# Optimization experiments

Hardware: AMD Instinct MI355X
Metric: run time of the kernel (lower is better)

The kernel has to match this reference:

```python
import jax, jax.numpy as jnp
import numpy as np

VOCAB = 32000
HID = 1024
HEADS = 16
HEAD_DIM = HID // HEADS
LAYERS = 8
INTER = 4 * HID
ROPE_BASE = 100000.0
EPS = 1e-5


def setup_inputs() -> dict:
    key = jax.random.key(0)
    ks = jax.random.split(key, 12)
    s = 0.02
    inp = {
        'input_ids': jax.random.randint(ks[0], (2, 2048), 0, VOCAB),
        'embed_W': jax.random.normal(ks[1], (VOCAB, HID), jnp.float32) * s,
        'Wq': jax.random.normal(ks[2], (LAYERS, HID, HID), jnp.float32) * s,
        'Wk': jax.random.normal(ks[3], (LAYERS, HID, HID), jnp.float32) * s,
        'Wv': jax.random.normal(ks[4], (LAYERS, HID, HID), jnp.float32) * s,
        'Wo': jax.random.normal(ks[5], (LAYERS, HID, HID), jnp.float32) * s,
        'Wg': jax.random.normal(ks[6], (LAYERS, HID, INTER), jnp.float32) * s,
        'Wu': jax.random.normal(ks[7], (LAYERS, HID, INTER), jnp.float32) * s,
        'Wd': jax.random.normal(ks[8], (LAYERS, INTER, HID), jnp.float32) * s,
        'norm1_w': jnp.ones((LAYERS, HID), jnp.float32),
        'norm2_w': jnp.ones((LAYERS, HID), jnp.float32),
        'final_norm_w': jnp.ones((HID,), jnp.float32),
        'head_W': jax.random.normal(ks[9], (HID, VOCAB), jnp.float32) * s,
    }
    return inp


def rms_norm(x, w):
    return x * jax.lax.rsqrt(jnp.mean(x * x, axis=-1, keepdims=True) + EPS) * w


def rope_tables(seq_len):
    freq = 1.0 / (ROPE_BASE ** (jnp.arange(0, HEAD_DIM, 2, dtype=jnp.float32) / HEAD_DIM))
    ang = jnp.arange(seq_len, dtype=jnp.float32)[:, None] * freq  # [S, d/2]
    cos = jnp.concatenate([jnp.cos(ang), jnp.cos(ang)], axis=-1)  # [S, d]
    sin = jnp.concatenate([jnp.sin(ang), jnp.sin(ang)], axis=-1)
    return cos, sin


def rotate_half(x):
    h = x.shape[-1] // 2
    return jnp.concatenate([-x[..., h:], x[..., :h]], axis=-1)


def apply_rope(q, k, cos, sin):
    # q,k: [B,S,H,D]; cos,sin: [S,D] -> broadcast over heads via [:,None,:]
    c = cos[:, None, :]
    s = sin[:, None, :]
    return q * c + rotate_half(q) * s, k * c + rotate_half(k) * s


def attention(x, wq, wk, wv, wo, cos, sin, causal_mask):
    B, S, _ = x.shape
    q = (x @ wq).reshape(B, S, HEADS, HEAD_DIM)
    k = (x @ wk).reshape(B, S, HEADS, HEAD_DIM)
    v = (x @ wv).reshape(B, S, HEADS, HEAD_DIM)
    q, k = apply_rope(q, k, cos, sin)
    scores = jnp.einsum('bqhd,bkhd->bhqk', q, k) / np.sqrt(HEAD_DIM)
    scores = jnp.clip(scores, -1000.0, 1000.0)
    scores = jnp.where(causal_mask, jnp.finfo(scores.dtype).min, scores)
    w = jax.nn.softmax(scores.astype(jnp.float32), axis=-1).astype(q.dtype)
    w = jnp.clip(w, 0.0, 1.0)
    ctx = jnp.einsum('bhqk,bkhd->bqhd', w, v).reshape(B, S, HID)
    return ctx @ wo


def reference(input_ids, embed_W, Wq, Wk, Wv, Wo, Wg, Wu, Wd, norm1_w, norm2_w, final_norm_w, head_W):
    B, S = input_ids.shape
    h = embed_W[input_ids]  # [B,S,HID]
    cos, sin = rope_tables(S)
    causal_mask = jnp.triu(jnp.ones((S, S), bool), k=1)[None, None]
    for l in range(LAYERS):
        h = h + attention(rms_norm(h, norm1_w[l]), Wq[l], Wk[l], Wv[l], Wo[l], cos, sin, causal_mask)
        hn = rms_norm(h, norm2_w[l])
        h = h + (jax.nn.silu(hn @ Wg[l]) * (hn @ Wu[l])) @ Wd[l]
    h = rms_norm(h, final_norm_w)
    logits = h @ head_W
    return logits, h
```

## Files before the change

### kernel.cpp

```cpp
#include <hip/hip_runtime.h>

#define T_TOK 4096
#define SEQ   2048
#define HID   1024
#define NH    16
#define HD    64
#define INTER 4096
#define NLAYER 8
#define VOCAB 32000

typedef short short8 __attribute__((ext_vector_type(8)));
typedef float f32x4  __attribute__((ext_vector_type(4)));

__device__ __forceinline__ unsigned short f2bf(float f){
  unsigned int u = __builtin_bit_cast(unsigned int, f);
  u += 0x7fffu + ((u >> 16) & 1u);
  return (unsigned short)(u >> 16);
}
__device__ __forceinline__ float bf2f(unsigned short b){
  unsigned int u = ((unsigned int)b) << 16;
  return __builtin_bit_cast(float, u);
}

#define GLOAD_LDS16(gsrc, ldst) \
  __builtin_amdgcn_global_load_lds((const __attribute__((address_space(1))) void*)(gsrc), \
                                   (__attribute__((address_space(3))) void*)(ldst), 16, 0, 0)

__global__ __launch_bounds__(256) void embed_kernel(const int* __restrict__ ids,
                                                    const float* __restrict__ W,
                                                    float* __restrict__ h){
  int i = blockIdx.x * 256 + threadIdx.x;
  int t = i >> 8, c = i & 255;
  ((float4*)h)[i] = ((const float4*)(W + (size_t)ids[t] * HID))[c];
}

__global__ __launch_bounds__(256) void rope_tab_kernel(float* __restrict__ cosT,
                                                       float* __restrict__ sinT){
  int i = blockIdx.x * 256 + threadIdx.x;
  int s = i >> 5, f = i & 31;
  float inv = expf(-((2.0f * (float)f) / 64.0f) * logf(100000.0f));
  float ang = (float)s * inv;
  cosT[i] = cosf(ang);
  sinT[i] = sinf(ang);
}

__global__ __launch_bounds__(256) void rmsnorm_kernel(const float* __restrict__ h,
                                                      const float* __restrict__ w,
                                                      unsigned short* __restrict__ out,
                                                      float* hcopy){
  int t = blockIdx.x, tid = threadIdx.x;
  float4 v = ((const float4*)(h + (size_t)t * HID))[tid];
  float ss = v.x*v.x + v.y*v.y + v.z*v.z + v.w*v.w;
  #pragma unroll
  for (int m = 1; m < 64; m <<= 1) ss += __shfl_xor(ss, m);
  __shared__ float red[4];
  if ((tid & 63) == 0) red[tid >> 6] = ss;
  __syncthreads();
  float r = rsqrtf((red[0] + red[1] + red[2] + red[3]) * (1.0f / HID) + 1e-5f);
  float4 wv = ((const float4*)w)[tid];
  float nx = v.x * r * wv.x;
  float ny = v.y * r * wv.y;
  float nz = v.z * r * wv.z;
  float nw = v.w * r * wv.w;
  ushort4 o;
  o.x = f2bf(nx); o.y = f2bf(ny); o.z = f2bf(nz); o.w = f2bf(nw);
  ((ushort4*)(out + (size_t)t * HID))[tid] = o;
  if (hcopy){
    float4 hv; hv.x = nx; hv.y = ny; hv.z = nz; hv.w = nw;
    ((float4*)(hcopy + (size_t)t * HID))[tid] = hv;
  }
}

__global__ __launch_bounds__(256) void rope_kernel(unsigned short* __restrict__ q,
                                                   unsigned short* __restrict__ k,
                                                   const float* __restrict__ cosT,
                                                   const float* __restrict__ sinT){
  int i = blockIdx.x * 256 + threadIdx.x;
  int t = i >> 9, rem = i & 511;
  int hh = rem >> 5, f = rem & 31;
  int s = t & (SEQ - 1);
  float c = cosT[s * 32 + f], sn = sinT[s * 32 + f];
  size_t base = (size_t)t * HID + hh * HD + f;
  float q0 = bf2f(q[base]), q1 = bf2f(q[base + 32]);
  q[base]      = f2bf((q0 * c - q1 * sn) * 0.125f);
  q[base + 32] = f2bf((q1 * c + q0 * sn) * 0.125f);
  float k0 = bf2f(k[base]), k1 = bf2f(k[base + 32]);
  k[base]      = f2bf(k0 * c - k1 * sn);
  k[base + 32] = f2bf(k1 * c + k0 * sn);
}

__global__ __launch_bounds__(256) void convert_w_swz(const float* __restrict__ W,
                                                     unsigned short* __restrict__ Wt,
                                                     int K, int N){
  __shared__ unsigned short t_lds[64][72];
  W  += (size_t)blockIdx.z * K * N;
  Wt += (size_t)blockIdx.z * K * N;
  const int n0 = blockIdx.x * 64, k0 = blockIdx.y * 64;
  const int tid = threadIdx.x;
  const int tr = tid >> 4, tc = tid & 15;
  #pragma unroll
  for (int i = 0; i < 4; ++i){
    int kk = tr + i * 16;
    float4 v = *(const float4*)(W + (size_t)(k0 + kk) * N + n0 + tc * 4);
    t_lds[tc*4+0][kk] = f2bf(v.x);
    t_lds[tc*4+1][kk] = f2bf(v.y);
    t_lds[tc*4+2][kk] = f2bf(v.z);
    t_lds[tc*4+3][kk] = f2bf(v.w);
  }
  __syncthreads();
  const int n = tid >> 2, cp = tid & 3;
  #pragma unroll
  for (int j = 0; j < 2; ++j){
    int c = cp * 2 + j;
    uint4 d = *(const uint4*)(&t_lds[n][c * 8]);
    *(uint4*)(Wt + (size_t)(n0 + n) * K + k0 + ((c ^ (n & 7)) << 3)) = d;
  }
}

__global__ __launch_bounds__(256) void convert_w_lin(const float* __restrict__ W,
                                                     unsigned short* __restrict__ Wt,
                                                     int K, int N){
  __shared__ unsigned short t_lds[64][72];
  const int n0 = blockIdx.x * 64, k0 = blockIdx.y * 64;
  const int tid = threadIdx.x;
  const int tr = tid >> 4, tc = tid & 15;
  #pragma unroll
  for (int i = 0; i < 4; ++i){
    int kk = tr + i * 16;
    float4 v = *(const float4*)(W + (size_t)(k0 + kk) * N + n0 + tc * 4);
    t_lds[tc*4+0][kk] = f2bf(v.x);
    t_lds[tc*4+1][kk] = f2bf(v.y);
    t_lds[tc*4+2][kk] = f2bf(v.z);
    t_lds[tc*4+3][kk] = f2bf(v.w);
  }
  __syncthreads();
  const int n = tid >> 2, cp = tid & 3;
  #pragma unroll
  for (int j = 0; j < 2; ++j){
    int c = cp * 2 + j;
    uint4 d = *(const uint4*)(&t_lds[n][c * 8]);
    *(uint4*)(Wt + (size_t)(n0 + n) * K + k0 + c * 8) = d;
  }
}

__device__ __forceinline__ void gemm_core64(const unsigned short* __restrict__ A,
                                            const unsigned short* __restrict__ Bt,
                                            int K, int m0, int n0,
                                            unsigned short* As, unsigned short* Bs,
                                            f32x4 (&acc)[4][4]){
  const int tid = threadIdx.x;
  const int lane = tid & 63, w = tid >> 6;
  const int l15 = lane & 15, g = lane >> 4;
  const int lr = lane >> 3;
  const int lc = lane & 7;
  const int wr = w >> 1, wc = w & 1;
  const int axor = ((lc ^ lr) << 3);

  #pragma unroll
  for (int m = 0; m < 4; ++m)
    #pragma unroll
    for (int n = 0; n < 4; ++n)
      #pragma unroll
      for (int i = 0; i < 4; ++i) acc[m][n][i] = 0.0f;

  for (int kk = 0; kk < K; kk += 64){
    __syncthreads();
    #pragma unroll
    for (int i = 0; i < 4; ++i){
      int rb = (i * 4 + w) * 8;
      GLOAD_LDS16(A  + (size_t)(m0 + rb + lr) * K + kk + axor,      As + rb * 64);
      GLOAD_LDS16(Bt + (size_t)(n0 + rb + lr) * K + kk + (lc << 3), Bs + rb * 64);
    }
    __syncthreads();
    short8 a[4][2], b[4][2];
    const int x = l15 & 7;
    #pragma unroll
    for (int m = 0; m < 4; ++m){
      int row = wr * 64 + m * 16 + l15;
      a[m][0] = *(const short8*)(As + row * 64 + ((g       ^ x) << 3));
      a[m][1] = *(const short8*)(As + row * 64 + (((4 + g) ^ x) << 3));
    }
    #pragma unroll
    for (int n = 0; n < 4; ++n){
      int row = wc * 64 + n * 16 + l15;
      b[n][0] = *(const short8*)(Bs + row * 64 + ((g       ^ x) << 3));
      b[n][1] = *(const short8*)(Bs + row * 64 + (((4 + g) ^ x) << 3));
    }
    #pragma unroll
    for (int m = 0; m < 4; ++m)
      #pragma unroll
      for (int n = 0; n < 4; ++n){
        acc[m][n] = __builtin_amdgcn_mfma_f32_16x16x32_bf16(a[m][0], b[n][0], acc[m][n], 0, 0, 0);
        acc[m][n] = __builtin_amdgcn_mfma_f32_16x16x32_bf16(a[m][1], b[n][1], acc[m][n], 0, 0, 0);
      }
  }
}

__device__ __forceinline__ void gemm_core32(const unsigned short* __restrict__ A,
                                            const unsigned short* __restrict__ Bt,
                                            int K, int m0, int n0,
                                            unsigned short* As, unsigned short* Bs,
                                            f32x4 (&acc)[4][4]){
  const int tid = threadIdx.x;
  const int lane = tid & 63, w = tid >> 6;
  const int l15 = lane & 15, g = lane >> 4;
  const int wr = w >> 1, wc = w & 1;
  const int srow = lane >> 2;
  const int schunk = (((lane & 3) ^ ((srow >> 1) & 3)) << 3);
  const int sx = (l15 >> 1) & 3;

  #pragma unroll
  for (int m = 0; m < 4; ++m)
    #pragma unroll
    for (int n = 0; n < 4; ++n)
      #pragma unroll
      for (int i = 0; i < 4; ++i) acc[m][n][i] = 0.0f;

  for (int kk = 0; kk < K; kk += 32){
    __syncthreads();
    GLOAD_LDS16(A  + (size_t)(m0 +      w*16 + srow) * K + kk + schunk, As + (w*16) * 32);
    GLOAD_LDS16(A  + (size_t)(m0 + 64 + w*16 + srow) * K + kk + schunk, As + (64 + w*16) * 32);
    GLOAD_LDS16(Bt + (size_t)(n0 +      w*16 + srow) * K + kk + schunk, Bs + (w*16) * 32);
    GLOAD_LDS16(Bt + (size_t)(n0 + 64 + w*16 + srow) * K + kk + schunk, Bs + (64 + w*16) * 32);
    __syncthreads();
    short8 a[4], b[4];
    #pragma unroll
    for (int m = 0; m < 4; ++m)
      a[m] = *(const short8*)(As + (wr*64 + m*16 + l15) * 32 + ((g ^ sx) << 3));
    #pragma unroll
    for (int n = 0; n < 4; ++n)
      b[n] = *(const short8*)(Bs + (wc*64 + n*16 + l15) * 32 + ((g ^ sx) << 3));
    #pragma unroll
    for (int m = 0; m < 4; ++m)
      #pragma unroll
      for (int n = 0; n < 4; ++n)
        acc[m][n] = __builtin_amdgcn_mfma_f32_16x16x32_bf16(a[m], b[n], acc[m][n], 0, 0, 0);
  }
}

template<int MODE>
__device__ __forceinline__ void gemm_epi(const f32x4 (&acc)[4][4], void* Cout,
                                         const float* __restrict__ resid,
                                         int N, int m0, int n0, int ldt){
  const int tid = threadIdx.x;
  const int lane = tid & 63, w = tid >> 6;
  const int l15 = lane & 15, g = lane >> 4;
  const int wr = w >> 1, wc = w & 1;
  #pragma unroll
  for (int m = 0; m < 4; ++m){
    #pragma unroll
    for (int n = 0; n < 4; ++n){
      int row0 = m0 + wr * 64 + m * 16 + g * 4;
      int col  = n0 + wc * 64 + n * 16 + l15;
      #pragma unroll
      for (int i = 0; i < 4; ++i){
        float v = acc[m][n][i];
        if (MODE == 0){
          ((unsigned short*)Cout)[(size_t)(row0 + i) * N + col] = f2bf(v);
        } else if (MODE == 1){
          size_t idx = (size_t)(row0 + i) * N + col;
          ((float*)Cout)[idx] = resid[idx] + v;
        } else if (MODE == 2){
          ((unsigned short*)Cout)[(size_t)col * ldt + (row0 + i)] = f2bf(v);
        } else {
          __builtin_nontemporal_store(v, &((float*)Cout)[(size_t)(row0 + i) * N + col]);
        }
      }
    }
  }
}

template<int MODE>
__global__ __launch_bounds__(256) void gemm64_k(const unsigned short* __restrict__ A,
                                                const unsigned short* __restrict__ Bt,
                                                void* Cout, const float* resid,
                                                int K, int N, int ldt){
  __shared__ unsigned short As[128 * 64];
  __shared__ unsigned short Bs[128 * 64];
  f32x4 acc[4][4];
  gemm_core64(A, Bt, K, blockIdx.x * 128, blockIdx.y * 128, As, Bs, acc);
  gemm_epi<MODE>(acc, Cout, resid, N, blockIdx.x * 128, blockIdx.y * 128, ldt);
}

__global__ __launch_bounds__(256) void gemm_qkv(const unsigned short* __restrict__ A,
                                                const unsigned short* __restrict__ BtQ,
                                                const unsigned short* __restrict__ BtK,
                                                const unsigned short* __restrict__ BtV,
                                                unsigned short* qb, unsigned short* kb,
                                                unsigned short* vt){
  __shared__ unsigned short As[128 * 64];
  __shared__ unsigned short Bs[128 * 64];
  const int nb = blockIdx.y, sel = nb >> 3, n0 = (nb & 7) * 128;
  const unsigned short* Bt = (sel == 0) ? BtQ : (sel == 1) ? BtK : BtV;
  f32x4 acc[4][4];
  gemm_core64(A, Bt, HID, blockIdx.x * 128, n0, As, Bs, acc);
  if (sel == 0)      gemm_epi<0>(acc, qb, nullptr, HID, blockIdx.x * 128, n0, 0);
  else if (sel == 1) gemm_epi<0>(acc, kb, nullptr, HID, blockIdx.x * 128, n0, 0);
  else               gemm_epi<2>(acc, vt, nullptr, HID, blockIdx.x * 128, n0, T_TOK);
}

__global__ __launch_bounds__(256) void gemm_gu(const unsigned short* __restrict__ A,
                                               const unsigned short* __restrict__ BtG,
                                               const unsigned short* __restrict__ BtU,
                                               unsigned short* gb, unsigned short* ub){
  __shared__ unsigned short As[128 * 64];
  __shared__ unsigned short Bs[128 * 64];
  const int nb = blockIdx.y, sel = nb >> 5, n0 = (nb & 31) * 128;
  f32x4 acc[4][4];
  gemm_core64(A, sel ? BtU : BtG, HID, blockIdx.x * 128, n0, As, Bs, acc);
  gemm_epi<0>(acc, sel ? ub : gb, nullptr, INTER, blockIdx.x * 128, n0, 0);
}

__global__ __launch_bounds__(256) void gemm_head(const unsigned short* __restrict__ A,
                                                 const unsigned short* __restrict__ Bt,
                                                 float* __restrict__ out){
  __shared__ unsigned short As[128 * 32];
  __shared__ unsigned short Bs[128 * 32];
  const int m0 = blockIdx.y * 128, n0 = blockIdx.x * 128;
  f32x4 acc[4][4];
  gemm_core32(A, Bt, HID, m0, n0, As, Bs, acc);
  gemm_epi<3>(acc, out, nullptr, VOCAB, m0, n0, 0);
}

__global__ __launch_bounds__(256, 2) void gemm_f32b(const unsigned short* __restrict__ A,
                                                    const float* __restrict__ Bw,
                                                    float* __restrict__ Cout,
                                                    int M, int N, int K){
  __shared__ unsigned short As[128 * 32];
  __shared__ unsigned short Bs[128 * 32];
  const int tid = threadIdx.x;
  const int lane = tid & 63, wid = tid >> 6;
  const int l15 = lane & 15, g = lane >> 4;
  const int wr = wid >> 1, wc = wid & 1;
  const int m0 = blockIdx.x * 128, n0 = blockIdx.y * 128;
  const int bcol = tid & 127, bhalf = tid >> 7;
  f32x4 acc[4][4];
  #pragma unroll
  for (int m = 0; m < 4; ++m)
    #pragma unroll
    for (int n = 0; n < 4; ++n)
      #pragma unroll
      for (int i = 0; i < 4; ++i) acc[m][n][i] = 0.0f;
  for (int kk = 0; kk < K; kk += 32){
    __syncthreads();
    #pragma unroll
    for (int cc = 0; cc < 2; ++cc){
      int c = tid + cc * 256;
      int row = c >> 2, kc = (c & 3) << 3;
      uint4 d = *(const uint4*)(A + (size_t)(m0 + row) * K + kk + kc);
      *(uint4*)(&As[row * 32 + kc]) = d;
    }
    {
      const float* bp = Bw + (size_t)(kk + bhalf * 16) * N + n0 + bcol;
      float f[16];
      #pragma unroll
      for (int j = 0; j < 16; ++j) f[j] = bp[(size_t)j * N];
      unsigned int pk[8];
      #pragma unroll
      for (int j = 0; j < 8; ++j)
        pk[j] = (unsigned int)f2bf(f[2*j]) | ((unsigned int)f2bf(f[2*j+1]) << 16);
      int sw = (bcol >> 1) & 3;
      int c0 = ((bhalf << 1)     ) ^ sw;
      int c1 = ((bhalf << 1) | 1 ) ^ sw;
      uint4 w0; w0.x = pk[0]; w0.y = pk[1]; w0.z = pk[2]; w0.w = pk[3];
      uint4 w1; w1.x = pk[4]; w1.y = pk[5]; w1.z = pk[6]; w1.w = pk[7];
      *(uint4*)(&Bs[bcol * 32 + c0 * 8]) = w0;
      *(uint4*)(&Bs[bcol * 32 + c1 * 8]) = w1;
    }
    __syncthreads();
    short8 a[4], b[4];
    #pragma unroll
    for (int m = 0; m < 4; ++m)
      a[m] = *(const short8*)(&As[(wr*64 + m*16 + l15) * 32 + g*8]);
    #pragma unroll
    for (int n = 0; n < 4; ++n){
      int col = wc*64 + n*16 + l15;
      b[n] = *(const short8*)(&Bs[col * 32 + (g ^ ((col >> 1) & 3)) * 8]);
    }
    #pragma unroll
    for (int m = 0; m < 4; ++m)
      #pragma unroll
      for (int n = 0; n < 4; ++n)
        acc[m][n] = __builtin_amdgcn_mfma_f32_16x16x32_bf16(a[m], b[n], acc[m][n], 0, 0, 0);
  }
  #pragma unroll
  for (int m = 0; m < 4; ++m)
    #pragma unroll
    for (int n = 0; n < 4; ++n){
      int row0 = m0 + wr*64 + m*16 + g*4;
      int col  = n0 + wc*64 + n*16 + l15;
      #pragma unroll
      for (int i = 0; i < 4; ++i)
        Cout[(size_t)(row0 + i) * N + col] = acc[m][n][i];
    }
}

__global__ __launch_bounds__(256) void attn_kernel(const unsigned short* __restrict__ q,
                                                   const unsigned short* __restrict__ k,
                                                   const unsigned short* __restrict__ vt,
                                                   unsigned short* __restrict__ ctx){
  const int tid = threadIdx.x;
  const int lane = tid & 63, w = tid >> 6;
  const int l15 = lane & 15, g = lane >> 4;
  const int bx = (int)gridDim.x - 1 - (int)blockIdx.x;
  const int q0 = bx * 128 + w * 32;
  const int hh = blockIdx.y;
  const int tb = blockIdx.z * SEQ;

  __shared__ unsigned short Ks[64][72];
  __shared__ unsigned short Vs[64][72];
  __shared__ unsigned short Ps[4][16][72];

  short8 qa[2][2];
  #pragma unroll
  for (int qs = 0; qs < 2; ++qs)
    #pragma unroll
    for (int kd = 0; kd < 2; ++kd)
      qa[qs][kd] = *(const short8*)(q + (size_t)(tb + q0 + qs*16 + l15) * HID + hh*HD + kd*32 + g*8);

  float m_run[2][4], l_run[2][4];
  f32x4 o_acc[2][4];
  #pragma unroll
  for (int qs = 0; qs < 2; ++qs)
    #pragma unroll
    for (int i = 0; i < 4; ++i){ m_run[qs][i] = -1e30f; l_run[qs][i] = 0.0f; }
  #pragma unroll
  for (int qs = 0; qs < 2; ++qs)
    #pragma unroll
    for (int dt = 0; dt < 4; ++dt)
      #pragma unroll
      for (int i = 0; i < 4; ++i) o_acc[qs][dt][i] = 0.0f;

  const int ntile = 2 * bx + 2;
  const int srow = tid >> 2, sc = (tid & 3) * 16;
  const unsigned short* kbase = k  + (size_t)(tb + srow) * HID + hh*HD + sc;
  const unsigned short* vbase = vt + (size_t)(hh*HD + srow) * T_TOK + tb + sc;

  for (int kt = 0; kt < ntile; ++kt){
    const int kv0 = kt * 64;
    __syncthreads();
    {
      const unsigned short* kp = kbase + (size_t)kv0 * HID;
      const unsigned short* vp = vbase + kv0;
      *(uint4*)(&Ks[srow][sc])     = *(const uint4*)(kp);
      *(uint4*)(&Ks[srow][sc + 8]) = *(const uint4*)(kp + 8);
      *(uint4*)(&Vs[srow][sc])     = *(const uint4*)(vp);
      *(uint4*)(&Vs[srow][sc + 8]) = *(const uint4*)(vp + 8);
    }
    __syncthreads();
    const int nct = min(4, ((q0 + 31 - kv0) >> 4) + 1);
    if (nct <= 0) continue;
    const int nks = nct >> 1;

    #pragma unroll
    for (int qs = 0; qs < 2; ++qs){
      float pv[4][4];
      #pragma unroll
      for (int ct = 0; ct < 4; ++ct){
        if (ct < nct){
          f32x4 scv;
          #pragma unroll
          for (int i = 0; i < 4; ++i) scv[i] = 0.0f;
          scv = __builtin_amdgcn_mfma_f32_16x16x32_bf16(qa[qs][0],
                  *(const short8*)(&Ks[ct*16 + l15][g*8]), scv, 0, 0, 0);
          scv = __builtin_amdgcn_mfma_f32_16x16x32_bf16(qa[qs][1],
                  *(const short8*)(&Ks[ct*16 + l15][32 + g*8]), scv, 0, 0, 0);
          #pragma unroll
          for (int i = 0; i < 4; ++i){
            float s = fminf(fmaxf(scv[i], -1000.0f), 1000.0f);
            int row = q0 + qs*16 + g*4 + i;
            int col = kv0 + ct*16 + l15;
            pv[ct][i] = (col > row) ? -1e30f : s;
          }
        } else {
          #pragma unroll
          for (int i = 0; i < 4; ++i) pv[ct][i] = -1e30f;
        }
      }
      #pragma unroll
      for (int i = 0; i < 4; ++i){
        float mx = fmaxf(fmaxf(pv[0][i], pv[1][i]), fmaxf(pv[2][i], pv[3][i]));
        #pragma unroll
        for (int msk = 1; msk < 16; msk <<= 1) mx = fmaxf(mx, __shfl_xor(mx, msk));
        if (!__all(mx <= m_run[qs][i] + 8.0f)){
          float mnew = fmaxf(m_run[qs][i], mx);
          float scale = __expf(m_run[qs][i] - mnew);
          m_run[qs][i] = mnew;
          l_run[qs][i] *= scale;
          #pragma unroll
          for (int dt = 0; dt < 4; ++dt) o_acc[qs][dt][i] *= scale;
        }
        float psum = 0.0f;
        #pragma unroll
        for (int ct = 0; ct < 4; ++ct){
          if (ct < nct){
            float p = __expf(pv[ct][i] - m_run[qs][i]);
            pv[ct][i] = p; psum += p;
          } else pv[ct][i] = 0.0f;
        }
        #pragma unroll
        for (int msk = 1; msk < 16; msk <<= 1) psum += __shfl_xor(psum, msk);
        l_run[qs][i] += psum;
      }
      #pragma unroll
      for (int ct = 0; ct < 4; ++ct)
        if (ct < nct)
          #pragma unroll
          for (int i = 0; i < 4; ++i)
            Ps[w][g*4 + i][ct*16 + l15] = f2bf(pv[ct][i]);
      #pragma unroll
      for (int ks = 0; ks < 2; ++ks){
        if (ks < nks){
          short8 ap = *(const short8*)(&Ps[w][l15][ks*32 + g*8]);
          #pragma unroll
          for (int dt = 0; dt < 4; ++dt){
            short8 vb = *(const short8*)(&Vs[dt*16 + l15][ks*32 + g*8]);
            o_acc[qs][dt] = __builtin_amdgcn_mfma_f32_16x16x32_bf16(ap, vb, o_acc[qs][dt], 0, 0, 0);
          }
        }
      }
    }
  }
  #pragma unroll
  for (int qs = 0; qs < 2; ++qs)
    #pragma unroll
    for (int dt = 0; dt < 4; ++dt)
      #pragma unroll
      for (int i = 0; i < 4; ++i){
        float o = o_acc[qs][dt][i] / l_run[qs][i];
        ctx[(size_t)(tb + q0 + qs*16 + g*4 + i) * HID + hh*HD + dt*16 + l15] = f2bf(o);
      }
}

__global__ __launch_bounds__(256) void silu_mul_kernel(unsigned short* __restrict__ gbuf,
                                                       const unsigned short* __restrict__ ubuf){
  int i = blockIdx.x * 256 + threadIdx.x;
  ushort4 gv = ((const ushort4*)gbuf)[i];
  ushort4 uv = ((const ushort4*)ubuf)[i];
  ushort4 o;
  float x;
  x = bf2f(gv.x); o.x = f2bf((x / (1.0f + __expf(-x))) * bf2f(uv.x));
  x = bf2f(gv.y); o.y = f2bf((x / (1.0f + __expf(-x))) * bf2f(uv.y));
  x = bf2f(gv.z); o.z = f2bf((x / (1.0f + __expf(-x))) * bf2f(uv.z));
  x = bf2f(gv.w); o.w = f2bf((x / (1.0f + __expf(-x))) * bf2f(uv.w));
  ((ushort4*)gbuf)[i] = o;
}

extern "C" void kernel_launch(void* const* d_in, const int* in_sizes, int n_in,
                              void* d_out, int out_size, void* d_ws, size_t ws_size,
                              hipStream_t stream){
  const int*   ids    = (const int*)d_in[0];
  const float* embedW = (const float*)d_in[1];
  const float* Wq = (const float*)d_in[2];
  const float* Wk = (const float*)d_in[3];
  const float* Wv = (const float*)d_in[4];
  const float* Wo = (const float*)d_in[5];
  const float* Wg = (const float*)d_in[6];
  const float* Wu = (const float*)d_in[7];
  const float* Wd = (const float*)d_in[8];
  const float* n1 = (const float*)d_in[9];
  const float* n2 = (const float*)d_in[10];
  const float* nf = (const float*)d_in[11];
  const float* Wh = (const float*)d_in[12];
  float* out = (float*)d_out;

  char* scb = (char*)d_out;
  unsigned short* qb  = (unsigned short*)(scb + 0);
  unsigned short* kb  = (unsigned short*)(scb + 8388608);
  unsigned short* vtb = (unsigned short*)(scb + 16777216);
  unsigned short* ctx = (unsigned short*)(scb + 25165824);
  unsigned short* gb  = (unsigned short*)(scb + 33554432);
  unsigned short* ub  = (unsigned short*)(scb + 67108864);
  float* cosT = (float*)(scb + 100663296);
  float* sinT = (float*)(scb + 100925440);
  float* h_fallback   = (float*)(scb + 104857600);
  unsigned short* WtQ = (unsigned short*)(scb + 134217728);
  unsigned short* WtK = (unsigned short*)(scb + 150994944);
  unsigned short* WtV = (unsigned short*)(scb + 167772160);
  unsigned short* WtO = (unsigned short*)(scb + 184549376);
  unsigned short* WtG = (unsigned short*)(scb + 201326592);
  unsigned short* WtU = (unsigned short*)(scb + 268435456);
  unsigned short* WtD = (unsigned short*)(scb + 335544320);

  unsigned short* xn = (unsigned short*)d_ws;
  float* h = (ws_size >= 25165824u) ? (float*)((char*)d_ws + 8388608) : h_fallback;
  unsigned short* WhT = (ws_size >= 90701824u)
                      ? (unsigned short*)((char*)d_ws + 25165824) : nullptr;

  convert_w_swz<<<dim3(16, 16, 8), 256, 0, stream>>>(Wq, WtQ, HID, HID);
  convert_w_swz<<<dim3(16, 16, 8), 256, 0, stream>>>(Wk, WtK, HID, HID);
  convert_w_swz<<<dim3(16, 16, 8), 256, 0, stream>>>(Wv, WtV, HID, HID);
  convert_w_swz<<<dim3(16, 16, 8), 256, 0, stream>>>(Wo, WtO, HID, HID);
  convert_w_swz<<<dim3(64, 16, 8), 256, 0, stream>>>(Wg, WtG, HID, INTER);
  convert_w_swz<<<dim3(64, 16, 8), 256, 0, stream>>>(Wu, WtU, HID, INTER);
  convert_w_swz<<<dim3(16, 64, 8), 256, 0, stream>>>(Wd, WtD, INTER, HID);
  if (WhT)
    convert_w_lin<<<dim3(500, 16, 1), 256, 0, stream>>>(Wh, WhT, HID, VOCAB);

  embed_kernel<<<4096, 256, 0, stream>>>(ids, embedW, h);
  rope_tab_kernel<<<256, 256, 0, stream>>>(cosT, sinT);

  for (int l = 0; l < NLAYER; ++l){
    rmsnorm_kernel<<<4096, 256, 0, stream>>>(h, n1 + l*HID, xn, nullptr);
    gemm_qkv<<<dim3(32, 24), 256, 0, stream>>>(xn, WtQ + (size_t)l*HID*HID,
                                               WtK + (size_t)l*HID*HID,
                                               WtV + (size_t)l*HID*HID, qb, kb, vtb);
    rope_kernel<<<8192, 256, 0, stream>>>(qb, kb, cosT, sinT);
    attn_kernel<<<dim3(16, 16, 2), 256, 0, stream>>>(qb, kb, vtb, ctx);
    gemm64_k<1><<<dim3(32, 8), 256, 0, stream>>>(ctx, WtO + (size_t)l*HID*HID,
                                                 h, h, HID, HID, 0);
    rmsnorm_kernel<<<4096, 256, 0, stream>>>(h, n2 + l*HID, xn, nullptr);
    gemm_gu<<<dim3(32, 64), 256, 0, stream>>>(xn, WtG + (size_t)l*HID*INTER,
                                              WtU + (size_t)l*HID*INTER, gb, ub);
    silu_mul_kernel<<<16384, 256, 0, stream>>>(gb, ub);
    gemm64_k<1><<<dim3(32, 8), 256, 0, stream>>>(gb, WtD + (size_t)l*HID*INTER,
                                                 h, h, INTER, HID, 0);
  }

  rmsnorm_kernel<<<4096, 256, 0, stream>>>(h, nf, xn, out + 131072000);
  if (WhT)
    gemm_head<<<dim3(250, 32), 256, 0, stream>>>(xn, WhT, out);
  else
    gemm_f32b<<<dim3(32, 250), 256, 0, stream>>>(xn, Wh, out, T_TOK, VOCAB, HID);
}
```

Before: 4.027 ms.

## Fuse RoPE into QKV GEMM, widen attention blocks, vectorize SiLU, reorder head grid

Applies RoPE and the query scale inside the QKV GEMM epilogue, which removes the separate rope kernel and its extra read and write of q and k. The attention kernel goes to 512 threads with 16 query rows per wave instead of 32, which raises wave count and shrinks per-thread registers at the cost of more K/V tile reuse per wave. SiLU-mul now handles 8 elements per thread, and the LM head uses a generic 32-K GEMM with the grid transposed so M varies fastest. The fused epilogue does scattered per-element cos/sin loads and bf16 stores, which may be less coalesced than before.

```diff
diff --git a/kernel.cpp b/kernel.cpp
--- a/kernel.cpp
+++ b/kernel.cpp
@@ -71,24 +71,6 @@
   }
 }
 
-__global__ __launch_bounds__(256) void rope_kernel(unsigned short* __restrict__ q,
-                                                   unsigned short* __restrict__ k,
-                                                   const float* __restrict__ cosT,
-                                                   const float* __restrict__ sinT){
-  int i = blockIdx.x * 256 + threadIdx.x;
-  int t = i >> 9, rem = i & 511;
-  int hh = rem >> 5, f = rem & 31;
-  int s = t & (SEQ - 1);
-  float c = cosT[s * 32 + f], sn = sinT[s * 32 + f];
-  size_t base = (size_t)t * HID + hh * HD + f;
-  float q0 = bf2f(q[base]), q1 = bf2f(q[base + 32]);
-  q[base]      = f2bf((q0 * c - q1 * sn) * 0.125f);
-  q[base + 32] = f2bf((q1 * c + q0 * sn) * 0.125f);
-  float k0 = bf2f(k[base]), k1 = bf2f(k[base + 32]);
-  k[base]      = f2bf(k0 * c - k1 * sn);
-  k[base + 32] = f2bf(k1 * c + k0 * sn);
-}
-
 __global__ __launch_bounds__(256) void convert_w_swz(const float* __restrict__ W,
                                                      unsigned short* __restrict__ Wt,
                                                      int K, int N){
@@ -282,21 +264,61 @@
   gemm_epi<MODE>(acc, Cout, resid, N, blockIdx.x * 128, blockIdx.y * 128, ldt);
 }
 
+template<int MODE>
+__global__ __launch_bounds__(256) void gemm32_k(const unsigned short* __restrict__ A,
+                                                const unsigned short* __restrict__ Bt,
+                                                void* Cout, const float* resid,
+                                                int K, int N, int ldt){
+  __shared__ unsigned short As[128 * 32];
+  __shared__ unsigned short Bs[128 * 32];
+  f32x4 acc[4][4];
+  gemm_core32(A, Bt, K, blockIdx.x * 128, blockIdx.y * 128, As, Bs, acc);
+  gemm_epi<MODE>(acc, Cout, resid, N, blockIdx.x * 128, blockIdx.y * 128, ldt);
+}
+
 __global__ __launch_bounds__(256) void gemm_qkv(const unsigned short* __restrict__ A,
                                                 const unsigned short* __restrict__ BtQ,
                                                 const unsigned short* __restrict__ BtK,
                                                 const unsigned short* __restrict__ BtV,
                                                 unsigned short* qb, unsigned short* kb,
-                                                unsigned short* vt){
+                                                unsigned short* vt,
+                                                const float* __restrict__ cosT,
+                                                const float* __restrict__ sinT){
   __shared__ unsigned short As[128 * 64];
   __shared__ unsigned short Bs[128 * 64];
   const int nb = blockIdx.y, sel = nb >> 3, n0 = (nb & 7) * 128;
   const unsigned short* Bt = (sel == 0) ? BtQ : (sel == 1) ? BtK : BtV;
   f32x4 acc[4][4];
   gemm_core64(A, Bt, HID, blockIdx.x * 128, n0, As, Bs, acc);
-  if (sel == 0)      gemm_epi<0>(acc, qb, nullptr, HID, blockIdx.x * 128, n0, 0);
-  else if (sel == 1) gemm_epi<0>(acc, kb, nullptr, HID, blockIdx.x * 128, n0, 0);
-  else               gemm_epi<2>(acc, vt, nullptr, HID, blockIdx.x * 128, n0, T_TOK);
+  if (sel == 2){
+    gemm_epi<2>(acc, vt, nullptr, HID, blockIdx.x * 128, n0, T_TOK);
+    return;
+  }
+  unsigned short* outp = sel ? kb : qb;
+  const float qs = sel ? 1.0f : 0.125f;
+  const int tid = threadIdx.x;
+  const int lane = tid & 63, w = tid >> 6;
+  const int l15 = lane & 15, g = lane >> 4;
+  const int wr = w >> 1, wc = w & 1;
+  const int m0 = blockIdx.x * 128;
+  #pragma unroll
+  for (int m = 0; m < 4; ++m){
+    #pragma unroll
+    for (int n = 0; n < 2; ++n){
+      int row0 = m0 + wr * 64 + m * 16 + g * 4;
+      int col  = n0 + wc * 64 + n * 16 + l15;
+      int f    = (col & 63);
+      #pragma unroll
+      for (int i = 0; i < 4; ++i){
+        int t = row0 + i, s = t & (SEQ - 1);
+        float c  = cosT[s * 32 + f];
+        float sn = sinT[s * 32 + f];
+        float x0 = acc[m][n][i], x1 = acc[m][n + 2][i];
+        outp[(size_t)t * HID + col]      = f2bf((x0 * c - x1 * sn) * qs);
+        outp[(size_t)t * HID + col + 32] = f2bf((x1 * c + x0 * sn) * qs);
+      }
+    }
+  }
 }
 
 __global__ __launch_bounds__(256) void gemm_gu(const unsigned short* __restrict__ A,
@@ -311,17 +333,6 @@
   gemm_epi<0>(acc, sel ? ub : gb, nullptr, INTER, blockIdx.x * 128, n0, 0);
 }
 
-__global__ __launch_bounds__(256) void gemm_head(const unsigned short* __restrict__ A,
-                                                 const unsigned short* __restrict__ Bt,
-                                                 float* __restrict__ out){
-  __shared__ unsigned short As[128 * 32];
-  __shared__ unsigned short Bs[128 * 32];
-  const int m0 = blockIdx.y * 128, n0 = blockIdx.x * 128;
-  f32x4 acc[4][4];
-  gemm_core32(A, Bt, HID, m0, n0, As, Bs, acc);
-  gemm_epi<3>(acc, out, nullptr, VOCAB, m0, n0, 0);
-}
-
 __global__ __launch_bounds__(256, 2) void gemm_f32b(const unsigned short* __restrict__ A,
                                                     const float* __restrict__ Bw,
                                                     float* __restrict__ Cout,
@@ -395,7 +406,7 @@
     }
 }
 
-__global__ __launch_bounds__(256) void attn_kernel(const unsigned short* __restrict__ q,
+__global__ __launch_bounds__(512) void attn_kernel(const unsigned short* __restrict__ q,
                                                    const unsigned short* __restrict__ k,
                                                    const unsigned short* __restrict__ vt,
                                                    unsigned short* __restrict__ ctx){
@@ -403,147 +414,131 @@
   const int lane = tid & 63, w = tid >> 6;
   const int l15 = lane & 15, g = lane >> 4;
   const int bx = (int)gridDim.x - 1 - (int)blockIdx.x;
-  const int q0 = bx * 128 + w * 32;
+  const int q0 = bx * 128 + w * 16;
   const int hh = blockIdx.y;
   const int tb = blockIdx.z * SEQ;
 
   __shared__ unsigned short Ks[64][72];
   __shared__ unsigned short Vs[64][72];
-  __shared__ unsigned short Ps[4][16][72];
-
-  short8 qa[2][2];
-  #pragma unroll
-  for (int qs = 0; qs < 2; ++qs)
-    #pragma unroll
-    for (int kd = 0; kd < 2; ++kd)
-      qa[qs][kd] = *(const short8*)(q + (size_t)(tb + q0 + qs*16 + l15) * HID + hh*HD + kd*32 + g*8);
-
-  float m_run[2][4], l_run[2][4];
-  f32x4 o_acc[2][4];
-  #pragma unroll
-  for (int qs = 0; qs < 2; ++qs)
-    #pragma unroll
-    for (int i = 0; i < 4; ++i){ m_run[qs][i] = -1e30f; l_run[qs][i] = 0.0f; }
-  #pragma unroll
-  for (int qs = 0; qs < 2; ++qs)
-    #pragma unroll
-    for (int dt = 0; dt < 4; ++dt)
-      #pragma unroll
-      for (int i = 0; i < 4; ++i) o_acc[qs][dt][i] = 0.0f;
+  __shared__ unsigned short Ps[8][16][72];
+
+  short8 qa[2];
+  #pragma unroll
+  for (int kd = 0; kd < 2; ++kd)
+    qa[kd] = *(const short8*)(q + (size_t)(tb + q0 + l15) * HID + hh*HD + kd*32 + g*8);
+
+  float m_run[4], l_run[4];
+  f32x4 o_acc[4];
+  #pragma unroll
+  for (int i = 0; i < 4; ++i){ m_run[i] = -1e30f; l_run[i] = 0.0f; }
+  #pragma unroll
+  for (int dt = 0; dt < 4; ++dt)
+    #pragma unroll
+    for (int i = 0; i < 4; ++i) o_acc[dt][i] = 0.0f;
 
   const int ntile = 2 * bx + 2;
-  const int srow = tid >> 2, sc = (tid & 3) * 16;
+  const int srow = tid >> 3, sc = (tid & 7) * 8;
   const unsigned short* kbase = k  + (size_t)(tb + srow) * HID + hh*HD + sc;
   const unsigned short* vbase = vt + (size_t)(hh*HD + srow) * T_TOK + tb + sc;
 
   for (int kt = 0; kt < ntile; ++kt){
     const int kv0 = kt * 64;
     __syncthreads();
-    {
-      const unsigned short* kp = kbase + (size_t)kv0 * HID;
-      const unsigned short* vp = vbase + kv0;
-      *(uint4*)(&Ks[srow][sc])     = *(const uint4*)(kp);
-      *(uint4*)(&Ks[srow][sc + 8]) = *(const uint4*)(kp + 8);
-      *(uint4*)(&Vs[srow][sc])     = *(const uint4*)(vp);
-      *(uint4*)(&Vs[srow][sc + 8]) = *(const uint4*)(vp + 8);
-    }
-    __syncthreads();
-    const int nct = min(4, ((q0 + 31 - kv0) >> 4) + 1);
+    *(uint4*)(&Ks[srow][sc]) = *(const uint4*)(kbase + (size_t)kv0 * HID);
+    *(uint4*)(&Vs[srow][sc]) = *(const uint4*)(vbase + kv0);
+    __syncthreads();
+    const int dq = q0 + 15 - kv0;
+    const int nct = (dq < 0) ? 0 : min(4, (dq >> 4) + 1);
     if (nct <= 0) continue;
-    const int nks = nct >> 1;
-
-    #pragma unroll
-    for (int qs = 0; qs < 2; ++qs){
-      float pv[4][4];
+
+    float pv[4][4];
+    #pragma unroll
+    for (int ct = 0; ct < 4; ++ct){
+      if (ct < nct){
+        f32x4 scv;
+        #pragma unroll
+        for (int i = 0; i < 4; ++i) scv[i] = 0.0f;
+        scv = __builtin_amdgcn_mfma_f32_16x16x32_bf16(qa[0],
+                *(const short8*)(&Ks[ct*16 + l15][g*8]), scv, 0, 0, 0);
+        scv = __builtin_amdgcn_mfma_f32_16x16x32_bf16(qa[1],
+                *(const short8*)(&Ks[ct*16 + l15][32 + g*8]), scv, 0, 0, 0);
+        #pragma unroll
+        for (int i = 0; i < 4; ++i){
+          float s = fminf(fmaxf(scv[i], -1000.0f), 1000.0f);
+          int row = q0 + g*4 + i;
+          int col = kv0 + ct*16 + l15;
+          pv[ct][i] = (col > row) ? -1e30f : s;
+        }
+      } else {
+        #pragma unroll
+        for (int i = 0; i < 4; ++i) pv[ct][i] = -1e30f;
+      }
+    }
+    #pragma unroll
+    for (int i = 0; i < 4; ++i){
+      float mx = fmaxf(fmaxf(pv[0][i], pv[1][i]), fmaxf(pv[2][i], pv[3][i]));
+      #pragma unroll
+      for (int msk = 1; msk < 16; msk <<= 1) mx = fmaxf(mx, __shfl_xor(mx, msk));
+      if (!__all(mx <= m_run[i] + 8.0f)){
+        float mnew = fmaxf(m_run[i], mx);
+        float scale = __expf(m_run[i] - mnew);
+        m_run[i] = mnew;
+        l_run[i] *= scale;
+        #pragma unroll
+        for (int dt = 0; dt < 4; ++dt) o_acc[dt][i] *= scale;
+      }
+      float psum = 0.0f;
       #pragma unroll
       for (int ct = 0; ct < 4; ++ct){
         if (ct < nct){
-          f32x4 scv;
-          #pragma unroll
-          for (int i = 0; i < 4; ++i) scv[i] = 0.0f;
-          scv = __builtin_amdgcn_mfma_f32_16x16x32_bf16(qa[qs][0],
-                  *(const short8*)(&Ks[ct*16 + l15][g*8]), scv, 0, 0, 0);
-          scv = __builtin_amdgcn_mfma_f32_16x16x32_bf16(qa[qs][1],
-                  *(const short8*)(&Ks[ct*16 + l15][32 + g*8]), scv, 0, 0, 0);
-          #pragma unroll
-          for (int i = 0; i < 4; ++i){
-            float s = fminf(fmaxf(scv[i], -1000.0f), 1000.0f);
-            int row = q0 + qs*16 + g*4 + i;
-            int col = kv0 + ct*16 + l15;
-            pv[ct][i] = (col > row) ? -1e30f : s;
-          }
-        } else {
-          #pragma unroll
-          for (int i = 0; i < 4; ++i) pv[ct][i] = -1e30f;
+          float p = __expf(pv[ct][i] - m_run[i]);
+          pv[ct][i] = p; psum += p;
+        } else pv[ct][i] = 0.0f;
+      }
+      #pragma unroll
+      for (int msk = 1; msk < 16; msk <<= 1) psum += __shfl_xor(psum, msk);
+      l_run[i] += psum;
+    }
+    #pragma unroll
+    for (int ct = 0; ct < 4; ++ct)
+      #pragma unroll
+      for (int i = 0; i < 4; ++i)
+        Ps[w][g*4 + i][ct*16 + l15] = f2bf(pv[ct][i]);
+    const int nks = (nct + 1) >> 1;
+    #pragma unroll
+    for (int ks = 0; ks < 2; ++ks){
+      if (ks < nks){
+        short8 ap = *(const short8*)(&Ps[w][l15][ks*32 + g*8]);
+        #pragma unroll
+        for (int dt = 0; dt < 4; ++dt){
+          short8 vb = *(const short8*)(&Vs[dt*16 + l15][ks*32 + g*8]);
+          o_acc[dt] = __builtin_amdgcn_mfma_f32_16x16x32_bf16(ap, vb, o_acc[dt], 0, 0, 0);
         }
       }
-      #pragma unroll
-      for (int i = 0; i < 4; ++i){
-        float mx = fmaxf(fmaxf(pv[0][i], pv[1][i]), fmaxf(pv[2][i], pv[3][i]));
-        #pragma unroll
-        for (int msk = 1; msk < 16; msk <<= 1) mx = fmaxf(mx, __shfl_xor(mx, msk));
-        if (!__all(mx <= m_run[qs][i] + 8.0f)){
-          float mnew = fmaxf(m_run[qs][i], mx);
-          float scale = __expf(m_run[qs][i] - mnew);
-          m_run[qs][i] = mnew;
-          l_run[qs][i] *= scale;
-          #pragma unroll
-          for (int dt = 0; dt < 4; ++dt) o_acc[qs][dt][i] *= scale;
-        }
-        float psum = 0.0f;
-        #pragma unroll
-        for (int ct = 0; ct < 4; ++ct){
-          if (ct < nct){
-            float p = __expf(pv[ct][i] - m_run[qs][i]);
-            pv[ct][i] = p; psum += p;
-          } else pv[ct][i] = 0.0f;
-        }
-        #pragma unroll
-        for (int msk = 1; msk < 16; msk <<= 1) psum += __shfl_xor(psum, msk);
-        l_run[qs][i] += psum;
-      }
-      #pragma unroll
-      for (int ct = 0; ct < 4; ++ct)
-        if (ct < nct)
-          #pragma unroll
-          for (int i = 0; i < 4; ++i)
-            Ps[w][g*4 + i][ct*16 + l15] = f2bf(pv[ct][i]);
-      #pragma unroll
-      for (int ks = 0; ks < 2; ++ks){
-        if (ks < nks){
-          short8 ap = *(const short8*)(&Ps[w][l15][ks*32 + g*8]);
-          #pragma unroll
-          for (int dt = 0; dt < 4; ++dt){
-            short8 vb = *(const short8*)(&Vs[dt*16 + l15][ks*32 + g*8]);
-            o_acc[qs][dt] = __builtin_amdgcn_mfma_f32_16x16x32_bf16(ap, vb, o_acc[qs][dt], 0, 0, 0);
-          }
-        }
-      }
-    }
-  }
-  #pragma unroll
-  for (int qs = 0; qs < 2; ++qs)
-    #pragma unroll
-    for (int dt = 0; dt < 4; ++dt)
-      #pragma unroll
-      for (int i = 0; i < 4; ++i){
-        float o = o_acc[qs][dt][i] / l_run[qs][i];
-        ctx[(size_t)(tb + q0 + qs*16 + g*4 + i) * HID + hh*HD + dt*16 + l15] = f2bf(o);
-      }
+    }
+  }
+  #pragma unroll
+  for (int dt = 0; dt < 4; ++dt)
+    #pragma unroll
+    for (int i = 0; i < 4; ++i){
+      float o = o_acc[dt][i] / l_run[i];
+      ctx[(size_t)(tb + q0 + g*4 + i) * HID + hh*HD + dt*16 + l15] = f2bf(o);
+    }
 }
 
 __global__ __launch_bounds__(256) void silu_mul_kernel(unsigned short* __restrict__ gbuf,
                                                        const unsigned short* __restrict__ ubuf){
   int i = blockIdx.x * 256 + threadIdx.x;
-  ushort4 gv = ((const ushort4*)gbuf)[i];
-  ushort4 uv = ((const ushort4*)ubuf)[i];
-  ushort4 o;
-  float x;
-  x = bf2f(gv.x); o.x = f2bf((x / (1.0f + __expf(-x))) * bf2f(uv.x));
-  x = bf2f(gv.y); o.y = f2bf((x / (1.0f + __expf(-x))) * bf2f(uv.y));
-  x = bf2f(gv.z); o.z = f2bf((x / (1.0f + __expf(-x))) * bf2f(uv.z));
-  x = bf2f(gv.w); o.w = f2bf((x / (1.0f + __expf(-x))) * bf2f(uv.w));
-  ((ushort4*)gbuf)[i] = o;
+  short8 gv = ((const short8*)gbuf)[i];
+  short8 uv = ((const short8*)ubuf)[i];
+  short8 o;
+  #pragma unroll
+  for (int j = 0; j < 8; ++j){
+    float x = bf2f((unsigned short)gv[j]);
+    float u = bf2f((unsigned short)uv[j]);
+    o[j] = (short)f2bf((x / (1.0f + __expf(-x))) * u);
+  }
+  ((short8*)gbuf)[i] = o;
 }
 
 extern "C" void kernel_launch(void* const* d_in, const int* in_sizes, int n_in,
@@ -604,22 +599,22 @@
     rmsnorm_kernel<<<4096, 256, 0, stream>>>(h, n1 + l*HID, xn, nullptr);
     gemm_qkv<<<dim3(32, 24), 256, 0, stream>>>(xn, WtQ + (size_t)l*HID*HID,
                                                WtK + (size_t)l*HID*HID,
-                                               WtV + (size_t)l*HID*HID, qb, kb, vtb);
-    rope_kernel<<<8192, 256, 0, stream>>>(qb, kb, cosT, sinT);
-    attn_kernel<<<dim3(16, 16, 2), 256, 0, stream>>>(qb, kb, vtb, ctx);
+                                               WtV + (size_t)l*HID*HID, qb, kb, vtb,
+                                               cosT, sinT);
+    attn_kernel<<<dim3(16, 16, 2), 512, 0, stream>>>(qb, kb, vtb, ctx);
     gemm64_k<1><<<dim3(32, 8), 256, 0, stream>>>(ctx, WtO + (size_t)l*HID*HID,
                                                  h, h, HID, HID, 0);
     rmsnorm_kernel<<<4096, 256, 0, stream>>>(h, n2 + l*HID, xn, nullptr);
     gemm_gu<<<dim3(32, 64), 256, 0, stream>>>(xn, WtG + (size_t)l*HID*INTER,
                                               WtU + (size_t)l*HID*INTER, gb, ub);
-    silu_mul_kernel<<<16384, 256, 0, stream>>>(gb, ub);
+    silu_mul_kernel<<<8192, 256, 0, stream>>>(gb, ub);
     gemm64_k<1><<<dim3(32, 8), 256, 0, stream>>>(gb, WtD + (size_t)l*HID*INTER,
                                                  h, h, INTER, HID, 0);
   }
 
   rmsnorm_kernel<<<4096, 256, 0, stream>>>(h, nf, xn, out + 131072000);
   if (WhT)
-    gemm_head<<<dim3(250, 32), 256, 0, stream>>>(xn, WhT, out);
+    gemm32_k<3><<<dim3(32, 250), 256, 0, stream>>>(xn, WhT, out, nullptr, HID, VOCAB, 0);
   else
     gemm_f32b<<<dim3(32, 250), 256, 0, stream>>>(xn, Wh, out, T_TOK, VOCAB, HID);
 }
```

New measurement: 3.879 ms. 3.7% less time.
